# Kernel tuning notes

Hardware: AMD Instinct MI355X
Metric: run time of the kernel (lower is better)

## Reference

```python
import jax, jax.numpy as jnp
import numpy as np

N, E, F, FO = 50000, 800000, 64, 64
BN_EPS = 1e-5


def bn(x, g, b):
    # training-mode BatchNorm1d (biased variance over batch dim)
    mu = jnp.mean(x, axis=0)
    var = jnp.mean((x - mu) ** 2, axis=0)
    return (x - mu) * jax.lax.rsqrt(var + BN_EPS) * g + b


def setup_inputs() -> dict:
    key = jax.random.key(0)
    ks = iter(jax.random.split(key, 40))
    nrm = lambda shape: jax.random.normal(next(ks), shape, jnp.float32) * 0.05
    d = {}
    d["x"] = jax.random.normal(next(ks), (N, F), jnp.float32)
    d["edge_index"] = jax.random.randint(next(ks), (2, E), 0, N)
    d["edge_attr"] = jax.random.normal(next(ks), (E, F), jnp.float32)
    # BatchNorm affine params for norm_in_h / norm_in_v
    d["gh_w"] = jnp.ones((F,)); d["gh_b"] = jnp.zeros((F,))
    d["gv_w"] = jnp.ones((F,)); d["gv_b"] = jnp.zeros((F,))
    # PointConv learnable softmax temperature t
    d["t"] = jnp.ones((1,), jnp.float32)
    # mlp_p: [3F -> 2F -> F], no norm
    d["p_w1"] = nrm((3 * F, 2 * F)); d["p_b1"] = jnp.zeros((2 * F,))
    d["p_w2"] = nrm((2 * F, F)); d["p_b2"] = jnp.zeros((F,))
    # mlp_h: [2F -> 2F -> 2F -> 2F -> FO], batch norm on hidden layers
    for i in (1, 2, 3):
        d[f"h_w{i}"] = nrm((2 * F, 2 * F)); d[f"h_b{i}"] = jnp.zeros((2 * F,))
        d[f"h_g{i}"] = jnp.ones((2 * F,)); d[f"h_bb{i}"] = jnp.zeros((2 * F,))
    d["h_w4"] = nrm((2 * F, FO)); d["h_b4"] = jnp.zeros((FO,))
    # edge_mlp: ReLU -> Linear(2*FO+F, 2*FO) -> ReLU -> Linear(2*FO, FO)
    d["e_w1"] = nrm((2 * FO + F, 2 * FO)); d["e_b1"] = jnp.zeros((2 * FO,))
    d["e_w2"] = nrm((2 * FO, FO)); d["e_b2"] = jnp.zeros((FO,))
    return d


def reference(x, edge_index, edge_attr, gh_w, gh_b, gv_w, gv_b, t,
              p_w1, p_b1, p_w2, p_b2,
              h_w1, h_b1, h_g1, h_bb1,
              h_w2, h_b2, h_g2, h_bb2,
              h_w3, h_b3, h_g3, h_bb3,
              h_w4, h_b4,
              e_w1, e_b1, e_w2, e_b2):
    n = x.shape[0]
    src, dst = edge_index[0], edge_index[1]  # x_j = x[src], x_i = x[dst]
    h = jax.nn.relu(bn(x, gh_w, gh_b))
    v = jax.nn.relu(bn(edge_attr, gv_w, gv_b))
    # message: mlp_p(cat([x_i, x_j, edge_attr]))  [E, F]
    z = jnp.concatenate([h[dst], h[src], v], axis=-1)
    m = jax.nn.relu(z @ p_w1 + p_b1) @ p_w2 + p_b2
    # scatter-softmax over edges sharing the same target, per feature
    s = m * t
    mx = jax.ops.segment_max(s, dst, num_segments=n)
    e = jnp.exp(s - mx[dst])
    denom = jax.ops.segment_sum(e, dst, num_segments=n)
    alpha = e / denom[dst]
    msg = jax.ops.segment_sum(m * alpha, dst, num_segments=n)  # [N, F]
    # update: mlp_h(cat([x_r, msg]))
    u = jnp.concatenate([h, msg], axis=-1)
    u = jax.nn.relu(bn(u @ h_w1 + h_b1, h_g1, h_bb1))
    u = jax.nn.relu(bn(u @ h_w2 + h_b2, h_g2, h_bb2))
    u = jax.nn.relu(bn(u @ h_w3 + h_b3, h_g3, h_bb3))
    h_out = u @ h_w4 + h_b4  # [N, FO]
    # edge update: edge_mlp starts with ReLU on the concat
    ev = jax.nn.relu(jnp.concatenate([h_out[src], h_out[dst], v], axis=-1))
    v_out = jax.nn.relu(ev @ e_w1 + e_b1) @ e_w2 + e_b2  # [E, FO]
    return (h_out, v_out)
```

## Files before the change

kernel.cpp:

```cpp
#include <hip/hip_runtime.h>
#include <math.h>

#define NN 50000
#define NE 800000

typedef __attribute__((ext_vector_type(8))) unsigned short us8;
typedef __attribute__((ext_vector_type(8))) __bf16 bf8;
typedef __attribute__((ext_vector_type(4))) float f4;

__device__ __forceinline__ unsigned short f2bf(float f) {
  unsigned int u = __float_as_uint(f);
  unsigned int r = u + 0x7FFFu + ((u >> 16) & 1u);
  return (unsigned short)(r >> 16);
}
__device__ __forceinline__ float bf2f(unsigned short h) {
  return __uint_as_float(((unsigned int)h) << 16);
}
__device__ __forceinline__ f4 mfma16(us8 a, us8 b, f4 c) {
  return __builtin_amdgcn_mfma_f32_16x16x32_bf16(
      __builtin_bit_cast(bf8, a), __builtin_bit_cast(bf8, b), c, 0, 0, 0);
}
__device__ __forceinline__ uint2 pack4(float a, float b, float c, float d) {
  uint2 r;
  r.x = (unsigned)f2bf(a) | ((unsigned)f2bf(b) << 16);
  r.y = (unsigned)f2bf(c) | ((unsigned)f2bf(d) << 16);
  return r;
}

__global__ void prep_stats(const float* __restrict__ x, const float* __restrict__ ea,
                           float* __restrict__ pstat) {
  int b = blockIdx.x;
  int t = threadIdx.x;
  const float* srcp; int rows; int nblk, b0;
  if (b < 256) { srcp = x;  rows = NN; nblk = 256;  b0 = b; }
  else         { srcp = ea; rows = NE; nblk = 1024; b0 = b - 256; }
  int cg = (t & 15) * 4;
  int rs = t >> 4;
  float4 s = {0.f, 0.f, 0.f, 0.f}, q = {0.f, 0.f, 0.f, 0.f};
  for (int r = b0 * 64 + rs; r < rows; r += nblk * 64) {
    #pragma unroll
    for (int u = 0; u < 4; ++u) {
      int rr = r + u * 16;
      if (rr < rows) {
        float4 v = *(const float4*)(srcp + (size_t)rr * 64 + cg);
        s.x += v.x; s.y += v.y; s.z += v.z; s.w += v.w;
        q.x += v.x * v.x; q.y += v.y * v.y; q.z += v.z * v.z; q.w += v.w * v.w;
      }
    }
  }
  __shared__ float4 ls[256], lq[256];
  ls[t] = s; lq[t] = q;
  __syncthreads();
  if (rs == 0) {
    #pragma unroll
    for (int i = 1; i < 16; ++i) {
      float4 a = ls[i * 16 + t], z = lq[i * 16 + t];
      s.x += a.x; s.y += a.y; s.z += a.z; s.w += a.w;
      q.x += z.x; q.y += z.y; q.z += z.z; q.w += z.w;
    }
    *(float4*)&pstat[(size_t)b * 128 + cg] = s;
    *(float4*)&pstat[(size_t)b * 128 + 64 + cg] = q;
  }
}

__global__ void reduce_stats(const float* __restrict__ pstat,
                             const float* __restrict__ gh_w, const float* __restrict__ gh_b,
                             const float* __restrict__ gv_w, const float* __restrict__ gv_b,
                             float* __restrict__ sb) {
  int t = threadIdx.x;
  int col = t & 63, slot = t >> 6;
  int base = blockIdx.x ? 256 : 0;
  int n = blockIdx.x ? 1024 : 256;
  float s = 0.f, q = 0.f;
  for (int r = slot; r < n; r += 16) {
    s += pstat[(size_t)(base + r) * 128 + col];
    q += pstat[(size_t)(base + r) * 128 + 64 + col];
  }
  __shared__ float ls[1024], lq[1024];
  ls[t] = s; lq[t] = q;
  __syncthreads();
  if (slot == 0) {
    #pragma unroll
    for (int i = 1; i < 16; ++i) { s += ls[i * 64 + col]; q += lq[i * 64 + col]; }
    float inv = blockIdx.x ? (1.0f / NE) : (1.0f / NN);
    const float* gp = blockIdx.x ? gv_w : gh_w;
    const float* bp = blockIdx.x ? gv_b : gh_b;
    float mu = s * inv;
    float var = q * inv - mu * mu;
    float sc = gp[col] * rsqrtf(var + 1e-5f);
    int o = blockIdx.x ? 128 : 0;
    sb[o + col] = sc;
    sb[o + 64 + col] = bp[col] - mu * sc;
  }
}

__global__ void reduce_sb(const float* __restrict__ part,
                          const float* __restrict__ g, const float* __restrict__ b,
                          float* __restrict__ scale, float* __restrict__ bias) {
  int t = threadIdx.x;
  int col = t & 127, slot = t >> 7;
  float s = 0.f, q = 0.f;
  for (int r = slot; r < 782; r += 8) {
    s += part[(size_t)r * 256 + col];
    q += part[(size_t)r * 256 + 128 + col];
  }
  __shared__ float ls[1024], lq[1024];
  ls[t] = s; lq[t] = q;
  __syncthreads();
  if (slot == 0) {
    #pragma unroll
    for (int i = 1; i < 8; ++i) { s += ls[i * 128 + col]; q += lq[i * 128 + col]; }
    float mu = s * (1.0f / NN);
    float var = q * (1.0f / NN) - mu * mu;
    float sc = g[col] * rsqrtf(var + 1e-5f);
    scale[col] = sc;
    bias[col] = b[col] - mu * sc;
  }
}

__global__ void rank_count(const int* __restrict__ dst, int* __restrict__ cnt,
                           int* __restrict__ rank) {
  int e = blockIdx.x * 256 + threadIdx.x;
  rank[e] = atomicAdd(&cnt[dst[e]], 1);
}

__global__ void wprep(const float* __restrict__ p_w1, const float* __restrict__ e_w1,
                      const float* __restrict__ p_w2, const float* __restrict__ e_w2,
                      const float* __restrict__ h_w1, const float* __restrict__ h_w2,
                      const float* __restrict__ h_w3, const float* __restrict__ h_w4,
                      unsigned short* __restrict__ wpab, unsigned short* __restrict__ wqab,
                      unsigned short* __restrict__ w1c_p, unsigned short* __restrict__ w1c_e,
                      unsigned short* __restrict__ w2f_p, unsigned short* __restrict__ w2f_e,
                      unsigned short* __restrict__ hw1t, unsigned short* __restrict__ hw2t,
                      unsigned short* __restrict__ hw3t, unsigned short* __restrict__ hw4t) {
  int gi = blockIdx.x * 256 + threadIdx.x;
  if (gi < 32768) {
    const float* w = (gi < 16384) ? p_w1 : e_w1;
    unsigned short* o = (gi < 16384) ? wpab : wqab;
    int i = gi & 16383;
    int f = i >> 6, k = i & 63;
    int srcrow = k + ((f >> 7) << 6);
    o[i] = f2bf(w[(size_t)srcrow * 128 + (f & 127)]);
  } else if (gi < 49152) {
    int i = (gi - 32768) & 8191;
    const float* w = (gi < 40960) ? (p_w1 + 128 * 128) : (e_w1 + 128 * 128);
    unsigned short* o = (gi < 40960) ? w1c_p : w1c_e;
    int f = i >> 6, k = i & 63;
    o[i] = f2bf(w[(size_t)k * 128 + f]);
  } else if (gi < 65536) {
    int i = (gi - 49152) & 8191;
    const float* w = (gi < 57344) ? p_w2 : e_w2;
    unsigned short* o = (gi < 57344) ? w2f_p : w2f_e;
    int j = i & 7, lane = (i >> 3) & 63, frag = i >> 9;
    int kc = frag >> 2, mb = frag & 3;
    int l15 = lane & 15, g = lane >> 4;
    o[i] = f2bf(w[(size_t)(kc * 32 + g * 8 + j) * 64 + 16 * mb + l15]);
  } else if (gi < 114688) {
    int seg = (gi - 65536) >> 14;
    int i = (gi - 65536) & 16383;
    const float* w = (seg == 0) ? h_w1 : (seg == 1) ? h_w2 : h_w3;
    unsigned short* o = (seg == 0) ? hw1t : (seg == 1) ? hw2t : hw3t;
    int n = i >> 7, k = i & 127;
    o[i] = f2bf(w[(size_t)k * 128 + n]);
  } else if (gi < 122880) {
    int i = gi - 114688;
    int n = i >> 7, k = i & 127;
    hw4t[i] = f2bf(h_w4[(size_t)k * 64 + n]);
  }
}

__global__ void scan_part(const int* __restrict__ cnt, int* __restrict__ bsum) {
  __shared__ int ls[256];
  int i = blockIdx.x * 256 + threadIdx.x;
  ls[threadIdx.x] = (i < NN) ? cnt[i] : 0;
  __syncthreads();
  for (int d = 128; d > 0; d >>= 1) {
    if (threadIdx.x < d) ls[threadIdx.x] += ls[threadIdx.x + d];
    __syncthreads();
  }
  if (threadIdx.x == 0) bsum[blockIdx.x] = ls[0];
}

__global__ void scan_top(int* __restrict__ bsum) {
  __shared__ int ps[256];
  int t = threadIdx.x;
  int v = (t < 196) ? bsum[t] : 0;
  ps[t] = v;
  __syncthreads();
  for (int d = 1; d < 256; d <<= 1) {
    int tv = (t >= d) ? ps[t - d] : 0;
    __syncthreads();
    ps[t] += tv;
    __syncthreads();
  }
  if (t < 196) bsum[t] = ps[t] - v;
}

__global__ void scan_add(const int* __restrict__ cnt, const int* __restrict__ bsum,
                         int* __restrict__ off) {
  __shared__ int ps[256];
  int t = threadIdx.x;
  int i = blockIdx.x * 256 + t;
  int v = (i < NN) ? cnt[i] : 0;
  ps[t] = v;
  __syncthreads();
  for (int d = 1; d < 256; d <<= 1) {
    int tv = (t >= d) ? ps[t - d] : 0;
    __syncthreads();
    ps[t] += tv;
    __syncthreads();
  }
  if (i < NN) off[i] = bsum[blockIdx.x] + ps[t] - v;
  if (blockIdx.x == 0 && t == 0) off[NN] = NE;
}

__global__ void scatter_all(const float* __restrict__ ea, const float* __restrict__ sc,
                            const float* __restrict__ bi,
                            const int* __restrict__ srca, const int* __restrict__ dsta,
                            const int* __restrict__ off, const int* __restrict__ rank,
                            int* __restrict__ src_s, int* __restrict__ dst_s,
                            int* __restrict__ einv, unsigned short* __restrict__ vbf) {
  __shared__ int posl[256];
  int t = threadIdx.x;
  int e0 = blockIdx.x * 256;
  int e = e0 + t;
  int n = dsta[e];
  int pos = off[n] + rank[e];
  posl[t] = pos;
  src_s[pos] = srca[e];
  dst_s[pos] = n;
  einv[pos] = e;
  __syncthreads();
  #pragma unroll
  for (int it = 0; it < 8; ++it) {
    int task = it * 256 + t;
    int r = task >> 3, q = task & 7;
    int c8 = q * 8;
    const float4* px = (const float4*)(ea + (size_t)(e0 + r) * 64 + c8);
    float4 a = px[0], b2 = px[1];
    float4 s0 = *(const float4*)(sc + c8), s1 = *(const float4*)(sc + c8 + 4);
    float4 b0 = *(const float4*)(bi + c8),  b1 = *(const float4*)(bi + c8 + 4);
    unsigned short tmp[8];
    tmp[0] = f2bf(fmaxf(a.x * s0.x + b0.x, 0.f));
    tmp[1] = f2bf(fmaxf(a.y * s0.y + b0.y, 0.f));
    tmp[2] = f2bf(fmaxf(a.z * s0.z + b0.z, 0.f));
    tmp[3] = f2bf(fmaxf(a.w * s0.w + b0.w, 0.f));
    tmp[4] = f2bf(fmaxf(b2.x * s1.x + b1.x, 0.f));
    tmp[5] = f2bf(fmaxf(b2.y * s1.y + b1.y, 0.f));
    tmp[6] = f2bf(fmaxf(b2.z * s1.z + b1.z, 0.f));
    tmp[7] = f2bf(fmaxf(b2.w * s1.w + b1.w, 0.f));
    *(uint4*)(vbf + (size_t)posl[r] * 64 + c8) = *(uint4*)tmp;
  }
}

__global__ __launch_bounds__(256) void pab_gemm(
    const float* __restrict__ in, const float* __restrict__ sc,
    const float* __restrict__ bi, const unsigned short* __restrict__ WT,
    unsigned short* __restrict__ out, float* __restrict__ hout) {
  __shared__ __align__(16) unsigned short Ul[64 * 72];
  const int t = threadIdx.x;
  const int w = t >> 6, l = t & 63, g = l >> 4, l15 = l & 15;
  const int r0 = blockIdx.x * 64;

  #pragma unroll
  for (int it = 0; it < 2; ++it) {
    int idx = it * 256 + t;
    int r = idx >> 3, q = idx & 7;
    int row = r0 + r; int rr = row < NN ? row : NN - 1;
    float4 v = *(const float4*)(in + (size_t)rr * 64 + q * 8);
    float4 v2 = *(const float4*)(in + (size_t)rr * 64 + q * 8 + 4);
    float4 s0 = *(const float4*)(sc + q * 8), s1 = *(const float4*)(sc + q * 8 + 4);
    float4 c0 = *(const float4*)(bi + q * 8), c1 = *(const float4*)(bi + q * 8 + 4);
    v.x = fmaxf(v.x * s0.x + c0.x, 0.f);   v.y = fmaxf(v.y * s0.y + c0.y, 0.f);
    v.z = fmaxf(v.z * s0.z + c0.z, 0.f);   v.w = fmaxf(v.w * s0.w + c0.w, 0.f);
    v2.x = fmaxf(v2.x * s1.x + c1.x, 0.f); v2.y = fmaxf(v2.y * s1.y + c1.y, 0.f);
    v2.z = fmaxf(v2.z * s1.z + c1.z, 0.f); v2.w = fmaxf(v2.w * s1.w + c1.w, 0.f);
    unsigned short tmp[8];
    tmp[0] = f2bf(v.x);  tmp[1] = f2bf(v.y);  tmp[2] = f2bf(v.z);  tmp[3] = f2bf(v.w);
    tmp[4] = f2bf(v2.x); tmp[5] = f2bf(v2.y); tmp[6] = f2bf(v2.z); tmp[7] = f2bf(v2.w);
    *(uint4*)&Ul[r * 72 + q * 8] = *(uint4*)tmp;
    if (row < NN) {
      *(float4*)(hout + (size_t)row * 64 + q * 8) = v;
      *(float4*)(hout + (size_t)row * 64 + q * 8 + 4) = v2;
    }
  }
  us8 a[4][2];
  #pragma unroll
  for (int mm = 0; mm < 4; ++mm)
    #pragma unroll
    for (int kc = 0; kc < 2; ++kc)
      a[mm][kc] = *(const us8*)(WT + (size_t)(64 * w + 16 * mm + l15) * 64 + kc * 32 + g * 8);
  __syncthreads();

  f4 c[4][4];
  #pragma unroll
  for (int mm = 0; mm < 4; ++mm)
    #pragma unroll
    for (int nb = 0; nb < 4; ++nb)
      c[mm][nb] = (f4){0.f, 0.f, 0.f, 0.f};
  #pragma unroll
  for (int kc = 0; kc < 2; ++kc) {
    us8 bz[4];
    #pragma unroll
    for (int nb = 0; nb < 4; ++nb)
      bz[nb] = *(const us8*)&Ul[(16 * nb + l15) * 72 + kc * 32 + g * 8];
    #pragma unroll
    for (int mm = 0; mm < 4; ++mm)
      #pragma unroll
      for (int nb = 0; nb < 4; ++nb)
        c[mm][nb] = mfma16(a[mm][kc], bz[nb], c[mm][nb]);
  }
  #pragma unroll
  for (int mm = 0; mm < 4; ++mm)
    #pragma unroll
    for (int nb = 0; nb < 4; ++nb) {
      int row = r0 + 16 * nb + l15;
      if (row < NN) {
        int f0 = 64 * w + 16 * mm + 4 * g;
        int half = f0 >> 7;
        int f1 = f0 & 127;
        int pos = half * 128 + ((f1 >> 5) << 5) + (((f1 & 15) >> 2) << 3) + (((f1 >> 4) & 1) << 2);
        *(uint2*)(out + (size_t)row * 256 + pos) =
            pack4(c[mm][nb][0], c[mm][nb][1], c[mm][nb][2], c[mm][nb][3]);
      }
    }
}

template<int MODE>
__global__ __launch_bounds__(256, 4) void edge_mlp4(
    const unsigned short* __restrict__ vbf,
    const unsigned short* __restrict__ AB,
    const int* __restrict__ idx0, const int* __restrict__ idx1,
    const int* __restrict__ einv,
    const unsigned short* __restrict__ W1cT, const float* __restrict__ B1,
    const unsigned short* __restrict__ W2F, const float* __restrict__ B2,
    void* __restrict__ outv) {
  __shared__ __align__(16) unsigned short Hl[64 * 136];
  __shared__ __align__(16) unsigned short W2l[8192];
  const int t = threadIdx.x;
  const int w = t >> 6, l = t & 63, g = l >> 4, l15 = l & 15;
  int bid = blockIdx.x;
  {
    const int q = 12500 / 8, r = 12500 % 8;
    int x = bid % 8, j = bid / 8;
    bid = (x < r ? x * (q + 1) : r * (q + 1) + (x - r) * q) + j;
  }
  const size_t e0 = (size_t)bid * 64;

  uint4 ga0[4], ga1[4];
  #pragma unroll
  for (int nb = 0; nb < 4; ++nb) {
    size_t e = e0 + 16 * nb + l15;
    int n0 = idx0[e], n1 = idx1[e];
    ga0[nb] = *(const uint4*)(AB + (size_t)n0 * 256 + w * 32 + g * 8);
    ga1[nb] = *(const uint4*)(AB + (size_t)n1 * 256 + 128 + w * 32 + g * 8);
  }
  int orig = 0;
  if (MODE == 2) orig = einv[e0 + 16 * w + l15];
  #pragma unroll
  for (int i = 0; i < 4; ++i) {
    uint4 v = *(const uint4*)(W2F + (size_t)(t + 256 * i) * 8);
    *(uint4*)&W2l[(t + 256 * i) * 8] = v;
  }
  us8 a1[2][2];
  #pragma unroll
  for (int mm = 0; mm < 2; ++mm)
    #pragma unroll
    for (int kc = 0; kc < 2; ++kc)
      a1[mm][kc] = *(const us8*)(W1cT + (size_t)(32 * w + 16 * mm + l15) * 64
                                 + kc * 32 + g * 8);

  f4 c1[2][4];
  #pragma unroll
  for (int mm = 0; mm < 2; ++mm)
    #pragma unroll
    for (int nb = 0; nb < 4; ++nb)
      c1[mm][nb] = (f4){0.f, 0.f, 0.f, 0.f};
  #pragma unroll
  for (int kc = 0; kc < 2; ++kc) {
    us8 bz[4];
    #pragma unroll
    for (int nb = 0; nb < 4; ++nb)
      bz[nb] = *(const us8*)(vbf + (e0 + 16 * nb + l15) * 64 + kc * 32 + g * 8);
    #pragma unroll
    for (int mm = 0; mm < 2; ++mm)
      #pragma unroll
      for (int nb = 0; nb < 4; ++nb)
        c1[mm][nb] = mfma16(a1[mm][kc], bz[nb], c1[mm][nb]);
  }

  #pragma unroll
  for (int mm = 0; mm < 2; ++mm) {
    float4 bb = *(const float4*)(B1 + 32 * w + 16 * mm + 4 * g);
    #pragma unroll
    for (int nb = 0; nb < 4; ++nb) {
      f4 v = c1[mm][nb];
      unsigned int ux = mm ? ga0[nb].z : ga0[nb].x;
      unsigned int uy = mm ? ga0[nb].w : ga0[nb].y;
      unsigned int vx = mm ? ga1[nb].z : ga1[nb].x;
      unsigned int vy = mm ? ga1[nb].w : ga1[nb].y;
      float h0 = v[0] + bb.x + bf2f((unsigned short)(ux & 0xffff))
                             + bf2f((unsigned short)(vx & 0xffff));
      float h1 = v[1] + bb.y + bf2f((unsigned short)(ux >> 16))
                             + bf2f((unsigned short)(vx >> 16));
      float h2 = v[2] + bb.z + bf2f((unsigned short)(uy & 0xffff))
                             + bf2f((unsigned short)(vy & 0xffff));
      float h3 = v[3] + bb.w + bf2f((unsigned short)(uy >> 16))
                             + bf2f((unsigned short)(vy >> 16));
      int er = 16 * nb + l15;
      *(uint2*)&Hl[er * 136 + 32 * w + 16 * mm + 4 * g] =
          pack4(fmaxf(h0, 0.f), fmaxf(h1, 0.f), fmaxf(h2, 0.f), fmaxf(h3, 0.f));
    }
  }
  __syncthreads();

  f4 c2[4];
  #pragma unroll
  for (int mb = 0; mb < 4; ++mb) {
    float4 bb = *(const float4*)(B2 + 16 * mb + 4 * g);
    c2[mb] = (f4){bb.x, bb.y, bb.z, bb.w};
  }
  #pragma unroll
  for (int kc = 0; kc < 4; ++kc) {
    us8 bh = *(const us8*)&Hl[(16 * w + l15) * 136 + kc * 32 + g * 8];
    #pragma unroll
    for (int mb = 0; mb < 4; ++mb) {
      us8 a2 = *(const us8*)&W2l[((kc * 4 + mb) * 64 + l) * 8];
      c2[mb] = mfma16(a2, bh, c2[mb]);
    }
  }

  if (MODE == 1) {
    size_t e = e0 + 16 * w + l15;
    #pragma unroll
    for (int mb = 0; mb < 4; ++mb)
      *(uint2*)((unsigned short*)outv + e * 64 + 16 * mb + 4 * g) =
          pack4(c2[mb][0], c2[mb][1], c2[mb][2], c2[mb][3]);
  } else {
    #pragma unroll
    for (int mb = 0; mb < 4; ++mb)
      *(float4*)((float*)outv + (size_t)orig * 64 + 16 * mb + 4 * g) =
          (float4){c2[mb][0], c2[mb][1], c2[mb][2], c2[mb][3]};
  }
}

template<int MODE, int OUTW, bool OUTBF, bool STATS>
__global__ __launch_bounds__(256) void node_mfma(
    const void* __restrict__ in0v, const float* __restrict__ in1,
    const float* __restrict__ sc, const float* __restrict__ bi,
    const unsigned short* __restrict__ WT, const float* __restrict__ B,
    void* __restrict__ yv, float* __restrict__ part) {
  __shared__ __align__(16) unsigned short Ul[64 * 136];
  const int t = threadIdx.x;
  const int w = t >> 6, l = t & 63, g = l >> 4, l15 = l & 15;
  const int r0 = blockIdx.x * 64;
  constexpr int NMB = OUTW / 64;

  {
    int r = t >> 2, q = t & 3;
    int row = r0 + r;
    int rr = row < NN ? row : NN - 1;
    unsigned short tmp[32];
    if (MODE == 0) {
      const float* base = (q < 2) ? (const float*)in0v : in1;
      const float4* p = (const float4*)(base + (size_t)rr * 64 + (q & 1) * 32);
      #pragma unroll
      for (int i = 0; i < 8; ++i) {
        float4 v = p[i];
        tmp[4*i+0] = f2bf(v.x); tmp[4*i+1] = f2bf(v.y);
        tmp[4*i+2] = f2bf(v.z); tmp[4*i+3] = f2bf(v.w);
      }
    } else {
      const unsigned short* srcp = (const unsigned short*)in0v + (size_t)rr * 128 + q * 32;
      #pragma unroll
      for (int i = 0; i < 4; ++i) {
        uint4 u = *(const uint4*)(srcp + i * 8);
        const unsigned short* us = (const unsigned short*)&u;
        #pragma unroll
        for (int j2 = 0; j2 < 2; ++j2) {
          int cb = q * 32 + i * 8 + j2 * 4;
          float4 s = *(const float4*)(sc + cb);
          float4 b = *(const float4*)(bi + cb);
          tmp[i*8+j2*4+0] = f2bf(fmaxf(bf2f(us[j2*4+0]) * s.x + b.x, 0.f));
          tmp[i*8+j2*4+1] = f2bf(fmaxf(bf2f(us[j2*4+1]) * s.y + b.y, 0.f));
          tmp[i*8+j2*4+2] = f2bf(fmaxf(bf2f(us[j2*4+2]) * s.z + b.z, 0.f));
          tmp[i*8+j2*4+3] = f2bf(fmaxf(bf2f(us[j2*4+3]) * s.w + b.w, 0.f));
        }
      }
    }
    unsigned short* ur = &Ul[r * 136 + q * 32];
    #pragma unroll
    for (int i = 0; i < 4; ++i)
      *(uint4*)&ur[i * 8] = *(uint4*)(tmp + i * 8);
  }

  __syncthreads();

  f4 c[NMB][4];
  #pragma unroll
  for (int mm = 0; mm < NMB; ++mm) {
    float4 bb = *(const float4*)(B + 16 * (NMB * w + mm) + 4 * g);
    #pragma unroll
    for (int nb = 0; nb < 4; ++nb)
      c[mm][nb] = (f4){bb.x, bb.y, bb.z, bb.w};
  }

  #pragma unroll
  for (int kc = 0; kc < 4; ++kc) {
    us8 bu[4];
    #pragma unroll
    for (int nb = 0; nb < 4; ++nb)
      bu[nb] = *(const us8*)&Ul[(16 * nb + l15) * 136 + kc * 32 + g * 8];
    #pragma unroll
    for (int mm = 0; mm < NMB; ++mm) {
      us8 a = *(const us8*)(WT + (size_t)(16 * (NMB * w + mm) + l15) * 128
                            + kc * 32 + g * 8);
      #pragma unroll
      for (int nb = 0; nb < 4; ++nb)
        c[mm][nb] = mfma16(a, bu[nb], c[mm][nb]);
    }
  }

  #pragma unroll
  for (int mm = 0; mm < NMB; ++mm)
    #pragma unroll
    for (int nb = 0; nb < 4; ++nb) {
      int row = r0 + l15 + 16 * nb;
      if (row < NN) {
        int f0 = 16 * (NMB * w + mm) + 4 * g;
        if (OUTBF) {
          *(uint2*)((unsigned short*)yv + (size_t)row * OUTW + f0) =
              pack4(c[mm][nb][0], c[mm][nb][1], c[mm][nb][2], c[mm][nb][3]);
        } else {
          *(float4*)((float*)yv + (size_t)row * OUTW + f0) =
              (float4){c[mm][nb][0], c[mm][nb][1], c[mm][nb][2], c[mm][nb][3]};
        }
      }
    }

  if (STATS) {
    float msk[4];
    #pragma unroll
    for (int nb = 0; nb < 4; ++nb)
      msk[nb] = (r0 + 16 * nb + l15 < NN) ? 1.f : 0.f;
    #pragma unroll
    for (int mm = 0; mm < NMB; ++mm) {
      float sv[4], qv[4];
      #pragma unroll
      for (int r = 0; r < 4; ++r) {
        float s = 0.f, q = 0.f;
        #pragma unroll
        for (int nb = 0; nb < 4; ++nb) {
          float v = c[mm][nb][r] * msk[nb];
          s += v; q += v * v;
        }
        #pragma unroll
        for (int d = 1; d < 16; d <<= 1) {
          s += __shfl_xor(s, d);
          q += __shfl_xor(q, d);
        }
        sv[r] = s; qv[r] = q;
      }
      if (l15 == 0) {
        int f0 = 16 * (NMB * w + mm) + 4 * g;
        *(float4*)&part[(size_t)blockIdx.x * 256 + f0] =
            (float4){sv[0], sv[1], sv[2], sv[3]};
        *(float4*)&part[(size_t)blockIdx.x * 256 + 128 + f0] =
            (float4){qv[0], qv[1], qv[2], qv[3]};
      }
    }
  }
}

__global__ __launch_bounds__(256) void node_last_qab(
    const unsigned short* __restrict__ in0, const float* __restrict__ sc,
    const float* __restrict__ bi,
    const unsigned short* __restrict__ WT, const float* __restrict__ B,
    const unsigned short* __restrict__ WQ,
    float* __restrict__ hout, unsigned short* __restrict__ QAB) {
  __shared__ __align__(16) unsigned short Ul[64 * 136];
  const int t = threadIdx.x;
  const int w = t >> 6, l = t & 63, g = l >> 4, l15 = l & 15;
  const int r0 = blockIdx.x * 64;

  {
    int r = t >> 2, q = t & 3;
    int row = r0 + r;
    int rr = row < NN ? row : NN - 1;
    unsigned short tmp[32];
    const unsigned short* srcp = in0 + (size_t)rr * 128 + q * 32;
    #pragma unroll
    for (int i = 0; i < 4; ++i) {
      uint4 u = *(const uint4*)(srcp + i * 8);
      const unsigned short* us = (const unsigned short*)&u;
      #pragma unroll
      for (int j2 = 0; j2 < 2; ++j2) {
        int cb = q * 32 + i * 8 + j2 * 4;
        float4 s = *(const float4*)(sc + cb);
        float4 b = *(const float4*)(bi + cb);
        tmp[i*8+j2*4+0] = f2bf(fmaxf(bf2f(us[j2*4+0]) * s.x + b.x, 0.f));
        tmp[i*8+j2*4+1] = f2bf(fmaxf(bf2f(us[j2*4+1]) * s.y + b.y, 0.f));
        tmp[i*8+j2*4+2] = f2bf(fmaxf(bf2f(us[j2*4+2]) * s.z + b.z, 0.f));
        tmp[i*8+j2*4+3] = f2bf(fmaxf(bf2f(us[j2*4+3]) * s.w + b.w, 0.f));
      }
    }
    unsigned short* ur = &Ul[r * 136 + q * 32];
    #pragma unroll
    for (int i = 0; i < 4; ++i)
      *(uint4*)&ur[i * 8] = *(uint4*)(tmp + i * 8);
  }

  __syncthreads();

  f4 c[4];
  {
    float4 bb = *(const float4*)(B + 16 * w + 4 * g);
    #pragma unroll
    for (int nb = 0; nb < 4; ++nb)
      c[nb] = (f4){bb.x, bb.y, bb.z, bb.w};
  }
  #pragma unroll
  for (int kc = 0; kc < 4; ++kc) {
    us8 bu[4];
    #pragma unroll
    for (int nb = 0; nb < 4; ++nb)
      bu[nb] = *(const us8*)&Ul[(16 * nb + l15) * 136 + kc * 32 + g * 8];
    us8 a = *(const us8*)(WT + (size_t)(16 * w + l15) * 128 + kc * 32 + g * 8);
    #pragma unroll
    for (int nb = 0; nb < 4; ++nb)
      c[nb] = mfma16(a, bu[nb], c[nb]);
  }

  #pragma unroll
  for (int nb = 0; nb < 4; ++nb) {
    int row = r0 + l15 + 16 * nb;
    if (row < NN) {
      int f0 = 16 * w + 4 * g;
      *(float4*)(hout + (size_t)row * 64 + f0) =
          (float4){c[nb][0], c[nb][1], c[nb][2], c[nb][3]};
    }
  }

  __syncthreads();
  #pragma unroll
  for (int nb = 0; nb < 4; ++nb) {
    *(uint2*)&Ul[(16 * nb + l15) * 72 + 16 * w + 4 * g] =
        pack4(fmaxf(c[nb][0], 0.f), fmaxf(c[nb][1], 0.f),
              fmaxf(c[nb][2], 0.f), fmaxf(c[nb][3], 0.f));
  }
  us8 aq[4][2];
  #pragma unroll
  for (int mm = 0; mm < 4; ++mm)
    #pragma unroll
    for (int kc = 0; kc < 2; ++kc)
      aq[mm][kc] = *(const us8*)(WQ + (size_t)(64 * w + 16 * mm + l15) * 64 + kc * 32 + g * 8);
  __syncthreads();

  f4 cq[4][4];
  #pragma unroll
  for (int mm = 0; mm < 4; ++mm)
    #pragma unroll
    for (int nb = 0; nb < 4; ++nb)
      cq[mm][nb] = (f4){0.f, 0.f, 0.f, 0.f};
  #pragma unroll
  for (int kc = 0; kc < 2; ++kc) {
    us8 bz[4];
    #pragma unroll
    for (int nb = 0; nb < 4; ++nb)
      bz[nb] = *(const us8*)&Ul[(16 * nb + l15) * 72 + kc * 32 + g * 8];
    #pragma unroll
    for (int mm = 0; mm < 4; ++mm)
      #pragma unroll
      for (int nb = 0; nb < 4; ++nb)
        cq[mm][nb] = mfma16(aq[mm][kc], bz[nb], cq[mm][nb]);
  }
  #pragma unroll
  for (int mm = 0; mm < 4; ++mm)
    #pragma unroll
    for (int nb = 0; nb < 4; ++nb) {
      int row = r0 + 16 * nb + l15;
      if (row < NN) {
        int f0 = 64 * w + 16 * mm + 4 * g;
        int half = f0 >> 7;
        int f1 = f0 & 127;
        int pos = half * 128 + ((f1 >> 5) << 5) + (((f1 & 15) >> 2) << 3) + (((f1 >> 4) & 1) << 2);
        *(uint2*)(QAB + (size_t)row * 256 + pos) =
            pack4(cq[mm][nb][0], cq[mm][nb][1], cq[mm][nb][2], cq[mm][nb][3]);
      }
    }
}

__global__ void node_softmax(const unsigned short* __restrict__ m,
                             const int* __restrict__ off,
                             const float* __restrict__ tptr,
                             float* __restrict__ msg) {
  int gw = (blockIdx.x * 256 + threadIdx.x) >> 6;
  int lane = threadIdx.x & 63;
  if (gw >= NN) return;
  float t = tptr[0];
  int beg = off[gw], end = off[gw + 1];
  int len = end - beg;
  float M[4] = {-3e38f, -3e38f, -3e38f, -3e38f};
  float S[4] = {0.f, 0.f, 0.f, 0.f};
  float W[4] = {0.f, 0.f, 0.f, 0.f};
  int i = beg;
  for (; i + 3 < end; i += 4) {
    float v0 = bf2f(m[(size_t)(i + 0) * 64 + lane]);
    float v1 = bf2f(m[(size_t)(i + 1) * 64 + lane]);
    float v2 = bf2f(m[(size_t)(i + 2) * 64 + lane]);
    float v3 = bf2f(m[(size_t)(i + 3) * 64 + lane]);
    float s0 = v0 * t, s1 = v1 * t, s2 = v2 * t, s3 = v3 * t;
    float M0 = fmaxf(M[0], s0), M1 = fmaxf(M[1], s1);
    float M2 = fmaxf(M[2], s2), M3 = fmaxf(M[3], s3);
    float c0 = __expf(M[0] - M0), c1 = __expf(M[1] - M1);
    float c2 = __expf(M[2] - M2), c3 = __expf(M[3] - M3);
    float p0 = __expf(s0 - M0), p1 = __expf(s1 - M1);
    float p2 = __expf(s2 - M2), p3 = __expf(s3 - M3);
    S[0] = S[0] * c0 + p0;  W[0] = W[0] * c0 + v0 * p0;  M[0] = M0;
    S[1] = S[1] * c1 + p1;  W[1] = W[1] * c1 + v1 * p1;  M[1] = M1;
    S[2] = S[2] * c2 + p2;  W[2] = W[2] * c2 + v2 * p2;  M[2] = M2;
    S[3] = S[3] * c3 + p3;  W[3] = W[3] * c3 + v3 * p3;  M[3] = M3;
  }
  for (; i < end; ++i) {
    float v0 = bf2f(m[(size_t)i * 64 + lane]);
    float s0 = v0 * t;
    float M0 = fmaxf(M[0], s0);
    float c0 = __expf(M[0] - M0);
    float p0 = __expf(s0 - M0);
    S[0] = S[0] * c0 + p0;  W[0] = W[0] * c0 + v0 * p0;  M[0] = M0;
  }
  float Mn = fmaxf(fmaxf(M[0], M[1]), fmaxf(M[2], M[3]));
  float Sm = 0.f, Wm = 0.f;
  #pragma unroll
  for (int k = 0; k < 4; ++k) {
    float ck = __expf(M[k] - Mn);
    Sm += S[k] * ck;
    Wm += W[k] * ck;
  }
  msg[(size_t)gw * 64 + lane] = (len > 0) ? (Wm / Sm) : 0.f;
}

extern "C" void kernel_launch(void* const* d_in, const int* in_sizes, int n_in,
                              void* d_out, int out_size, void* d_ws, size_t ws_size,
                              hipStream_t stream) {
  const float* x     = (const float*)d_in[0];
  const int*   ei    = (const int*)d_in[1];
  const float* ea    = (const float*)d_in[2];
  const float* gh_w  = (const float*)d_in[3];
  const float* gh_b  = (const float*)d_in[4];
  const float* gv_w  = (const float*)d_in[5];
  const float* gv_b  = (const float*)d_in[6];
  const float* tpar  = (const float*)d_in[7];
  const float* p_w1  = (const float*)d_in[8];
  const float* p_b1  = (const float*)d_in[9];
  const float* p_w2  = (const float*)d_in[10];
  const float* p_b2  = (const float*)d_in[11];
  const float* h_w1  = (const float*)d_in[12];
  const float* h_b1  = (const float*)d_in[13];
  const float* h_g1  = (const float*)d_in[14];
  const float* h_bb1 = (const float*)d_in[15];
  const float* h_w2  = (const float*)d_in[16];
  const float* h_b2  = (const float*)d_in[17];
  const float* h_g2  = (const float*)d_in[18];
  const float* h_bb2 = (const float*)d_in[19];
  const float* h_w3  = (const float*)d_in[20];
  const float* h_b3  = (const float*)d_in[21];
  const float* h_g3  = (const float*)d_in[22];
  const float* h_bb3 = (const float*)d_in[23];
  const float* h_w4  = (const float*)d_in[24];
  const float* h_b4  = (const float*)d_in[25];
  const float* e_w1  = (const float*)d_in[26];
  const float* e_b1  = (const float*)d_in[27];
  const float* e_w2  = (const float*)d_in[28];
  const float* e_b2  = (const float*)d_in[29];

  float* h_out = (float*)d_out;
  float* v_out = (float*)d_out + (size_t)NN * 64;

  const int* src = ei;
  const int* dst = ei + NE;

  char* w = (char*)d_ws;
  int* cnt = (int*)w;
  size_t zero_bytes = 200704;

  char* p = w + zero_bytes;
  float* sb = (float*)p; p += 4096;
  float* sbx_s = sb,       *sbx_b = sb + 64;
  float* sbv_s = sb + 128, *sbv_b = sb + 192;
  float* sb1_s = sb + 256, *sb1_b = sb + 384;
  float* sb2_s = sb + 512, *sb2_b = sb + 640;
  float* sb3_s = sb + 768, *sb3_b = sb + 896;
  float* pstat = (float*)p; p += 1280 * 128 * 4;
  float* npart = (float*)p; p += 782 * 256 * 4;
  int* bsum   = (int*)p; p += 1024;
  int* off    = (int*)p; p += 200704;
  int* rank   = (int*)p; p += (size_t)NE * 4;
  int* einv   = (int*)p; p += (size_t)NE * 4;
  int* src_s  = (int*)p; p += (size_t)NE * 4;
  int* dst_s  = (int*)p; p += (size_t)NE * 4;
  float* h    = (float*)p; p += (size_t)NN * 64 * 4;
  float* msg  = (float*)p; p += (size_t)NN * 64 * 4;
  unsigned short* vbf  = (unsigned short*)p; p += (size_t)NE * 64 * 2;
  unsigned short* m_bf = (unsigned short*)p; p += (size_t)NE * 64 * 2;
  unsigned short* PAB  = (unsigned short*)p; p += (size_t)NN * 256 * 2;
  unsigned short* QAB  = (unsigned short*)p; p += (size_t)NN * 256 * 2;
  unsigned short* y1   = (unsigned short*)p; p += (size_t)NN * 128 * 2;
  unsigned short* y2   = (unsigned short*)p; p += (size_t)NN * 128 * 2;
  unsigned short* wpab  = (unsigned short*)p; p += 256 * 64 * 2;
  unsigned short* wqab  = (unsigned short*)p; p += 256 * 64 * 2;
  unsigned short* w1c_p = (unsigned short*)p; p += 128 * 64 * 2;
  unsigned short* w1c_e = (unsigned short*)p; p += 128 * 64 * 2;
  unsigned short* w2f_p = (unsigned short*)p; p += 64 * 128 * 2;
  unsigned short* w2f_e = (unsigned short*)p; p += 64 * 128 * 2;
  unsigned short* h_w1t = (unsigned short*)p; p += 128 * 128 * 2;
  unsigned short* h_w2t = (unsigned short*)p; p += 128 * 128 * 2;
  unsigned short* h_w3t = (unsigned short*)p; p += 128 * 128 * 2;
  unsigned short* h_w4t = (unsigned short*)p; p += 64 * 128 * 2;

  hipMemsetAsync(d_ws, 0, zero_bytes, stream);

  wprep<<<480, 256, 0, stream>>>(p_w1, e_w1, p_w2, e_w2, h_w1, h_w2, h_w3, h_w4,
                                 wpab, wqab, w1c_p, w1c_e, w2f_p, w2f_e,
                                 h_w1t, h_w2t, h_w3t, h_w4t);

  prep_stats<<<1280, 256, 0, stream>>>(x, ea, pstat);

  rank_count<<<3125, 256, 0, stream>>>(dst, cnt, rank);

  scan_part<<<196, 256, 0, stream>>>(cnt, bsum);
  scan_top<<<1, 256, 0, stream>>>(bsum);
  scan_add<<<196, 256, 0, stream>>>(cnt, bsum, off);

  reduce_stats<<<2, 1024, 0, stream>>>(pstat, gh_w, gh_b, gv_w, gv_b, sb);

  scatter_all<<<3125, 256, 0, stream>>>(ea, sbv_s, sbv_b, src, dst, off, rank,
                                        src_s, dst_s, einv, vbf);

  pab_gemm<<<782, 256, 0, stream>>>(x, sbx_s, sbx_b, wpab, PAB, h);

  edge_mlp4<1><<<12500, 256, 0, stream>>>(vbf, PAB, dst_s, src_s, einv,
                                          w1c_p, p_b1, w2f_p, p_b2, (void*)m_bf);

  node_softmax<<<12500, 256, 0, stream>>>(m_bf, off, tpar, msg);

  node_mfma<0, 128, true, true><<<782, 256, 0, stream>>>(
      h, msg, nullptr, nullptr, h_w1t, h_b1, (void*)y1, npart);
  reduce_sb<<<1, 1024, 0, stream>>>(npart, h_g1, h_bb1, sb1_s, sb1_b);

  node_mfma<1, 128, true, true><<<782, 256, 0, stream>>>(
      y1, nullptr, sb1_s, sb1_b, h_w2t, h_b2, (void*)y2, npart);
  reduce_sb<<<1, 1024, 0, stream>>>(npart, h_g2, h_bb2, sb2_s, sb2_b);

  node_mfma<1, 128, true, true><<<782, 256, 0, stream>>>(
      y2, nullptr, sb2_s, sb2_b, h_w3t, h_b3, (void*)y1, npart);
  reduce_sb<<<1, 1024, 0, stream>>>(npart, h_g3, h_bb3, sb3_s, sb3_b);

  node_last_qab<<<782, 256, 0, stream>>>(y1, sb3_s, sb3_b, h_w4t, h_b4, wqab,
                                         h_out, QAB);

  edge_mlp4<2><<<12500, 256, 0, stream>>>(vbf, QAB, src_s, dst_s, einv,
                                          w1c_e, e_b1, w2f_e, e_b2, (void*)v_out);
}
```

Baseline: 713.6 us.

## Merge offset scan into one kernel and widen edge MLP blocks to 128 edges

Replaces the three-kernel prefix scan over node degree counts with a single 1024-thread block that does a serial per-thread chunk sum, a shared-memory scan, and a serial write-back. This removes two kernel launches. The edge MLP kernel now runs 512-thread blocks that each handle two 64-edge groups sharing one W2 copy in LDS, which halves the per-edge weight staging and the block count. In exchange, the single-block scan is serial per thread, and the larger LDS footprint and the launch bounds change may limit occupancy.

```diff
diff --git a/kernel.cpp b/kernel.cpp
--- a/kernel.cpp
+++ b/kernel.cpp
@@ -169,49 +169,25 @@
   }
 }
 
-__global__ void scan_part(const int* __restrict__ cnt, int* __restrict__ bsum) {
-  __shared__ int ls[256];
-  int i = blockIdx.x * 256 + threadIdx.x;
-  ls[threadIdx.x] = (i < NN) ? cnt[i] : 0;
-  __syncthreads();
-  for (int d = 128; d > 0; d >>= 1) {
-    if (threadIdx.x < d) ls[threadIdx.x] += ls[threadIdx.x + d];
+__global__ void scan_offsets(const int* __restrict__ cnt, int* __restrict__ off) {
+  __shared__ int ps[1024];
+  const int NPT = (NN + 1023) / 1024;
+  int t = threadIdx.x;
+  int base = t * NPT;
+  int end = base + NPT; if (end > NN) end = NN;
+  int s = 0;
+  for (int i = base; i < end; ++i) s += cnt[i];
+  ps[t] = s;
+  __syncthreads();
+  for (int d = 1; d < 1024; d <<= 1) {
+    int v = (t >= d) ? ps[t - d] : 0;
     __syncthreads();
-  }
-  if (threadIdx.x == 0) bsum[blockIdx.x] = ls[0];
-}
-
-__global__ void scan_top(int* __restrict__ bsum) {
-  __shared__ int ps[256];
-  int t = threadIdx.x;
-  int v = (t < 196) ? bsum[t] : 0;
-  ps[t] = v;
-  __syncthreads();
-  for (int d = 1; d < 256; d <<= 1) {
-    int tv = (t >= d) ? ps[t - d] : 0;
+    ps[t] += v;
     __syncthreads();
-    ps[t] += tv;
-    __syncthreads();
-  }
-  if (t < 196) bsum[t] = ps[t] - v;
-}
-
-__global__ void scan_add(const int* __restrict__ cnt, const int* __restrict__ bsum,
-                         int* __restrict__ off) {
-  __shared__ int ps[256];
-  int t = threadIdx.x;
-  int i = blockIdx.x * 256 + t;
-  int v = (i < NN) ? cnt[i] : 0;
-  ps[t] = v;
-  __syncthreads();
-  for (int d = 1; d < 256; d <<= 1) {
-    int tv = (t >= d) ? ps[t - d] : 0;
-    __syncthreads();
-    ps[t] += tv;
-    __syncthreads();
-  }
-  if (i < NN) off[i] = bsum[blockIdx.x] + ps[t] - v;
-  if (blockIdx.x == 0 && t == 0) off[NN] = NE;
+  }
+  int pre = t ? ps[t - 1] : 0;
+  for (int i = base; i < end; ++i) { off[i] = pre; pre += cnt[i]; }
+  if (t == 1023) off[NN] = NE;
 }
 
 __global__ void scatter_all(const float* __restrict__ ea, const float* __restrict__ sc,
@@ -327,7 +303,7 @@
 }
 
 template<int MODE>
-__global__ __launch_bounds__(256, 4) void edge_mlp4(
+__global__ __launch_bounds__(512, 6) void edge_mlp5(
     const unsigned short* __restrict__ vbf,
     const unsigned short* __restrict__ AB,
     const int* __restrict__ idx0, const int* __restrict__ idx1,
@@ -335,39 +311,40 @@
     const unsigned short* __restrict__ W1cT, const float* __restrict__ B1,
     const unsigned short* __restrict__ W2F, const float* __restrict__ B2,
     void* __restrict__ outv) {
-  __shared__ __align__(16) unsigned short Hl[64 * 136];
+  __shared__ __align__(16) unsigned short Hl[2][64 * 136];
   __shared__ __align__(16) unsigned short W2l[8192];
   const int t = threadIdx.x;
   const int w = t >> 6, l = t & 63, g = l >> 4, l15 = l & 15;
+  const int gi = w >> 2, w4 = w & 3;
   int bid = blockIdx.x;
   {
-    const int q = 12500 / 8, r = 12500 % 8;
+    const int q = 6250 / 8, r = 6250 % 8;
     int x = bid % 8, j = bid / 8;
     bid = (x < r ? x * (q + 1) : r * (q + 1) + (x - r) * q) + j;
   }
-  const size_t e0 = (size_t)bid * 64;
+  const size_t e0 = (size_t)bid * 128 + (size_t)gi * 64;
 
   uint4 ga0[4], ga1[4];
   #pragma unroll
   for (int nb = 0; nb < 4; ++nb) {
     size_t e = e0 + 16 * nb + l15;
     int n0 = idx0[e], n1 = idx1[e];
-    ga0[nb] = *(const uint4*)(AB + (size_t)n0 * 256 + w * 32 + g * 8);
-    ga1[nb] = *(const uint4*)(AB + (size_t)n1 * 256 + 128 + w * 32 + g * 8);
+    ga0[nb] = *(const uint4*)(AB + (size_t)n0 * 256 + w4 * 32 + g * 8);
+    ga1[nb] = *(const uint4*)(AB + (size_t)n1 * 256 + 128 + w4 * 32 + g * 8);
   }
   int orig = 0;
-  if (MODE == 2) orig = einv[e0 + 16 * w + l15];
-  #pragma unroll
-  for (int i = 0; i < 4; ++i) {
-    uint4 v = *(const uint4*)(W2F + (size_t)(t + 256 * i) * 8);
-    *(uint4*)&W2l[(t + 256 * i) * 8] = v;
+  if (MODE == 2) orig = einv[e0 + 16 * w4 + l15];
+  #pragma unroll
+  for (int i = 0; i < 2; ++i) {
+    int idx = t + 512 * i;
+    *(uint4*)&W2l[idx * 8] = *(const uint4*)(W2F + (size_t)idx * 8);
   }
   us8 a1[2][2];
   #pragma unroll
   for (int mm = 0; mm < 2; ++mm)
     #pragma unroll
     for (int kc = 0; kc < 2; ++kc)
-      a1[mm][kc] = *(const us8*)(W1cT + (size_t)(32 * w + 16 * mm + l15) * 64
+      a1[mm][kc] = *(const us8*)(W1cT + (size_t)(32 * w4 + 16 * mm + l15) * 64
                                  + kc * 32 + g * 8);
 
   f4 c1[2][4];
@@ -391,7 +368,7 @@
 
   #pragma unroll
   for (int mm = 0; mm < 2; ++mm) {
-    float4 bb = *(const float4*)(B1 + 32 * w + 16 * mm + 4 * g);
+    float4 bb = *(const float4*)(B1 + 32 * w4 + 16 * mm + 4 * g);
     #pragma unroll
     for (int nb = 0; nb < 4; ++nb) {
       f4 v = c1[mm][nb];
@@ -408,7 +385,7 @@
       float h3 = v[3] + bb.w + bf2f((unsigned short)(uy >> 16))
                              + bf2f((unsigned short)(vy >> 16));
       int er = 16 * nb + l15;
-      *(uint2*)&Hl[er * 136 + 32 * w + 16 * mm + 4 * g] =
+      *(uint2*)&Hl[gi][er * 136 + 32 * w4 + 16 * mm + 4 * g] =
           pack4(fmaxf(h0, 0.f), fmaxf(h1, 0.f), fmaxf(h2, 0.f), fmaxf(h3, 0.f));
     }
   }
@@ -422,7 +399,7 @@
   }
   #pragma unroll
   for (int kc = 0; kc < 4; ++kc) {
-    us8 bh = *(const us8*)&Hl[(16 * w + l15) * 136 + kc * 32 + g * 8];
+    us8 bh = *(const us8*)&Hl[gi][(16 * w4 + l15) * 136 + kc * 32 + g * 8];
     #pragma unroll
     for (int mb = 0; mb < 4; ++mb) {
       us8 a2 = *(const us8*)&W2l[((kc * 4 + mb) * 64 + l) * 8];
@@ -431,7 +408,7 @@
   }
 
   if (MODE == 1) {
-    size_t e = e0 + 16 * w + l15;
+    size_t e = e0 + 16 * w4 + l15;
     #pragma unroll
     for (int mb = 0; mb < 4; ++mb)
       *(uint2*)((unsigned short*)outv + e * 64 + 16 * mb + 4 * g) =
@@ -793,7 +770,6 @@
   float* sb3_s = sb + 768, *sb3_b = sb + 896;
   float* pstat = (float*)p; p += 1280 * 128 * 4;
   float* npart = (float*)p; p += 782 * 256 * 4;
-  int* bsum   = (int*)p; p += 1024;
   int* off    = (int*)p; p += 200704;
   int* rank   = (int*)p; p += (size_t)NE * 4;
   int* einv   = (int*)p; p += (size_t)NE * 4;
@@ -828,9 +804,7 @@
 
   rank_count<<<3125, 256, 0, stream>>>(dst, cnt, rank);
 
-  scan_part<<<196, 256, 0, stream>>>(cnt, bsum);
-  scan_top<<<1, 256, 0, stream>>>(bsum);
-  scan_add<<<196, 256, 0, stream>>>(cnt, bsum, off);
+  scan_offsets<<<1, 1024, 0, stream>>>(cnt, off);
 
   reduce_stats<<<2, 1024, 0, stream>>>(pstat, gh_w, gh_b, gv_w, gv_b, sb);
 
@@ -839,8 +813,8 @@
 
   pab_gemm<<<782, 256, 0, stream>>>(x, sbx_s, sbx_b, wpab, PAB, h);
 
-  edge_mlp4<1><<<12500, 256, 0, stream>>>(vbf, PAB, dst_s, src_s, einv,
-                                          w1c_p, p_b1, w2f_p, p_b2, (void*)m_bf);
+  edge_mlp5<1><<<6250, 512, 0, stream>>>(vbf, PAB, dst_s, src_s, einv,
+                                         w1c_p, p_b1, w2f_p, p_b2, (void*)m_bf);
 
   node_softmax<<<12500, 256, 0, stream>>>(m_bf, off, tpar, msg);
 
@@ -859,6 +833,6 @@
   node_last_qab<<<782, 256, 0, stream>>>(y1, sb3_s, sb3_b, h_w4t, h_b4, wqab,
                                          h_out, QAB);
 
-  edge_mlp4<2><<<12500, 256, 0, stream>>>(vbf, QAB, src_s, dst_s, einv,
-                                          w1c_e, e_b1, w2f_e, e_b2, (void*)v_out);
-}
+  edge_mlp5<2><<<6250, 512, 0, stream>>>(vbf, QAB, src_s, dst_s, einv,
+                                         w1c_e, e_b1, w2f_e, e_b2, (void*)v_out);
+}
```

Measured after the change: 904.7 us. +26.8%, slower.
